# Performance work log

Hardware: AMD Instinct MI355X
Metric: run time of the kernel (lower is better)

The kernel has to match this reference:

```python
import jax, jax.numpy as jnp
import numpy as np

N_ITER = 4  # n_iter
NEG = -1e9  # masked-score fill (softmax-safe stand-in for -inf)


def _mfvi(x, mask, ternary, global_):
    """MFVI message passing between head (H) and node (Z) variables with global nodes.

    x:       [B, L, D] unary scores for Z nodes
    mask:    [B, L]    padding mask (nonzero = valid token)
    ternary: [D, D, H] ternary factor scores f(Z_i=a, Z_j=b, H-channel c)
    global_: [G, D, H] global-node factor scores
    Defaults: norm=softmax, regularize=1, stepsize=1, damping=0, async_update,
    no tensor decomposition, mode='all-attn', block_msg=False, output_prob=False.
    """
    B, L, D = x.shape
    m1 = (mask != 0)                                             # [B, L]
    pair_valid = m1[:, None, :, None] & m1[:, None, None, :]     # [B, 1, L, L]
    unary = x                                                    # pos_embed='none'
    Qz = jax.nn.softmax(unary, axis=-1)                          # [B, L, D]
    F_Z = unary
    neg = jnp.asarray(NEG, x.dtype)
    for _ in range(N_ITER):
        # --- H update: scores for head variable H_{i,c} over candidate heads j ---
        # F_Hs[n,h,i,j] = sum_{a,b} Qz[n,i,a] * ternary[a,b,h] * Qz[n,j,b]
        F_Hs = jnp.einsum('nia,abh,njb->nhij', Qz, ternary, Qz)  # [B, H, L, L]
        F_Hs = jnp.where(pair_valid, F_Hs, neg)
        # global-node columns: F_Hg[n,h,i,g] = sum_a Qz[n,i,a] * global_[g,a,h]
        F_Hg = jnp.einsum('nia,gah->nhig', Qz, global_)          # [B, H, L, G]
        F_H = jnp.concatenate([F_Hs, F_Hg], axis=-1)             # [B, H, L, L+G]
        Q_H = jax.nn.softmax(F_H, axis=-1)                       # regularize_H = 1
        Qhs, Qhg = Q_H[..., :L], Q_H[..., L:]
        # --- Z update (async: uses fresh Q_H) ---
        # message to Z_i from its chosen head j
        msg_i = jnp.einsum('nhij,njb,abh->nia', Qhs, Qz, ternary)
        # message to Z_j from dependents i (block_msg=False keeps it)
        msg_j = jnp.einsum('nhij,nia,abh->njb', Qhs, Qz, ternary)
        # message to Z_i from global nodes
        msg_g = jnp.einsum('nhig,gah->nia', Qhg, global_)
        F_Z = unary + msg_i + msg_j + msg_g                      # [B, L, D]
        Qz = jax.nn.softmax(F_Z, axis=-1)                        # regularize_Z = 1
    # output_prob=False -> unnormalized scores, zeroed at padding
    return jnp.where(m1[..., None], F_Z, jnp.zeros_like(F_Z))


def setup_inputs() -> dict:
    key = jax.random.key(0)
    k1, k2, k3 = jax.random.split(key, 3)
    B, L, D, H, G = 4, 1024, 128, 8, 64
    x = jax.random.normal(k1, (B, L, D), dtype=jnp.float32)
    mask = jnp.ones((B, L), dtype=jnp.int32)
    ternary = jax.random.normal(k2, (D, D, H), dtype=jnp.float32)          # init std=1
    global_ = jax.random.normal(k3, (G, D, H), dtype=jnp.float32) / np.sqrt(D)
    return {"x": x, "mask": mask, "ternary": ternary, "global_": global_}


def reference(x, mask, ternary, global_):
    return _mfvi(x, mask, ternary, global_)
```

## Files before the change

kernel.cpp:

```cpp
#include <hip/hip_runtime.h>
#include <math.h>

#define Bn 4
#define Ln 1024
#define Dn 128
#define Hn 8
#define Gn 64
#define NITERS 4

typedef _Float16 f16;
typedef _Float16 half8 __attribute__((ext_vector_type(8)));
typedef _Float16 half4v __attribute__((ext_vector_type(4)));
typedef float floatx4 __attribute__((ext_vector_type(4)));

#define WPAD 136
#define PPAD 72

#define MFMA(a, b, c) __builtin_amdgcn_mfma_f32_16x16x32_f16((a), (b), (c), 0, 0, 0)

__device__ __forceinline__ void gl_lds16(const f16* g, f16* l) {
    __builtin_amdgcn_global_load_lds(
        (const __attribute__((address_space(1))) void*)(g),
        (__attribute__((address_space(3))) void*)(l),
        16, 0, 0);
}

__device__ __forceinline__ void issue_tiles(const f16* us, const f16* ub, int sb,
                                            f16* UsB, f16* UbB, int w, int l) {
    #pragma unroll
    for (int k = 0; k < 4; k++) {
        int c = w * 4 + k;
        {
            int r = c * 4 + (l >> 4); int g = (l & 15) ^ (r & 7);
            gl_lds16(us + (size_t)r * Dn + g * 8, UsB + c * 512);
        }
        {
            int r = c * 8 + (l >> 3); int g = (l & 7) ^ (r & 7);
            gl_lds16(ub + (size_t)r * sb + g * 8, UbB + c * 512);
        }
    }
}

__global__ void repack_kernel(const float* __restrict__ ter, const float* __restrict__ glb,
                              f16* __restrict__ TpA, f16* __restrict__ TpB,
                              f16* __restrict__ GpA, f16* __restrict__ Gpt) {
    int idx = blockIdx.x * 256 + threadIdx.x;
    if (idx < Dn * Dn * Hn) {
        int h = idx % Hn; int b = (idx / Hn) % Dn; int a = idx / (Hn * Dn);
        f16 v = (f16)ter[idx];
        TpA[((size_t)h * Dn + a) * Dn + b] = v;
        TpB[((size_t)h * Dn + b) * Dn + a] = v;
    }
    if (idx < Gn * Dn * Hn) {
        int h = idx % Hn; int a = (idx / Hn) % Dn; int g = idx / (Hn * Dn);
        f16 v = (f16)glb[idx];
        GpA[((size_t)h * Gn + g) * Dn + a] = v;
        Gpt[((size_t)h * Dn + a) * Gn + g] = v;
    }
}

__global__ void softmax_rows_kernel(const float* __restrict__ in, f16* __restrict__ out) {
    int row = blockIdx.x;
    int t = threadIdx.x;
    __shared__ float red[2];
    float v = in[(size_t)row * Dn + t];
    float m = v;
    #pragma unroll
    for (int off = 1; off < 64; off <<= 1) m = fmaxf(m, __shfl_xor(m, off, 64));
    if ((t & 63) == 0) red[t >> 6] = m;
    __syncthreads();
    m = fmaxf(red[0], red[1]);
    float e = __expf(v - m);
    float s = e;
    #pragma unroll
    for (int off = 1; off < 64; off <<= 1) s += __shfl_xor(s, off, 64);
    __syncthreads();
    if ((t & 63) == 0) red[t >> 6] = s;
    __syncthreads();
    s = red[0] + red[1];
    out[(size_t)row * Dn + t] = (f16)(e / s);
}

__launch_bounds__(256, 4)
__global__ void uv_kernel(const f16* __restrict__ Qz, const f16* __restrict__ TpA,
                          const f16* __restrict__ TpB,
                          f16* __restrict__ U, f16* __restrict__ Ut, f16* __restrict__ Vt) {
    int bx = blockIdx.x;
    int h  = blockIdx.y;
    int n  = blockIdx.z;
    int t  = threadIdx.x;
    int w = t >> 6, l = t & 63, m = l & 15, q = l >> 4;

    __shared__ __align__(16) f16 Ts[128 * WPAD];

    int jrow = bx * 64 + w * 16 + m;
    const f16* qbase = Qz + ((size_t)n * Ln + jrow) * Dn;
    half8 aq[4];
    #pragma unroll
    for (int ks = 0; ks < 4; ks++)
        aq[ks] = *(const half8*)(qbase + ks * 32 + q * 8);

    size_t hoff = (size_t)(n * Hn + h);
    int jr0 = bx * 64 + w * 16 + 4 * q;

    {
        const f16* src = TpA + (size_t)h * Dn * Dn;
        for (int ii = 0; ii < 8; ii++) {
            int idx = t + 256 * ii; int r = idx >> 4, c = idx & 15;
            *(float4*)&Ts[r * WPAD + c * 8] = *(const float4*)(src + (size_t)r * Dn + c * 8);
        }
        __syncthreads();
        #pragma unroll
        for (int ct = 0; ct < 8; ct++) {
            floatx4 acc = {0.f, 0.f, 0.f, 0.f};
            #pragma unroll
            for (int ks = 0; ks < 4; ks++) {
                half8 b = *(const half8*)&Ts[(ct * 16 + m) * WPAD + ks * 32 + q * 8];
                acc = MFMA(aq[ks], b, acc);
            }
            f16* ub = U + (hoff * Ln + jr0) * Dn + ct * 16 + m;
            #pragma unroll
            for (int reg = 0; reg < 4; reg++) ub[(size_t)reg * Dn] = (f16)acc[reg];
            half4v pk = { (f16)acc[0], (f16)acc[1], (f16)acc[2], (f16)acc[3] };
            *(half4v*)(Ut + (hoff * Dn + ct * 16 + m) * Ln + jr0) = pk;
        }
        __syncthreads();
    }
    {
        const f16* src = TpB + (size_t)h * Dn * Dn;
        for (int ii = 0; ii < 8; ii++) {
            int idx = t + 256 * ii; int r = idx >> 4, c = idx & 15;
            *(float4*)&Ts[r * WPAD + c * 8] = *(const float4*)(src + (size_t)r * Dn + c * 8);
        }
        __syncthreads();
        #pragma unroll
        for (int ct = 0; ct < 8; ct++) {
            floatx4 acc = {0.f, 0.f, 0.f, 0.f};
            #pragma unroll
            for (int ks = 0; ks < 4; ks++) {
                half8 b = *(const half8*)&Ts[(ct * 16 + m) * WPAD + ks * 32 + q * 8];
                acc = MFMA(aq[ks], b, acc);
            }
            half4v pk = { (f16)acc[0], (f16)acc[1], (f16)acc[2], (f16)acc[3] };
            *(half4v*)(Vt + (hoff * Dn + ct * 16 + m) * Ln + jr0) = pk;
        }
    }
}

__launch_bounds__(256, 2)
__global__ void msgi_kernel(const f16* __restrict__ Qz, const f16* __restrict__ U,
                            const f16* __restrict__ Ut, const f16* __restrict__ GpA,
                            const f16* __restrict__ Gpt, const int* __restrict__ mask,
                            f16* __restrict__ Macc, float* __restrict__ rowLinv) {
    int it = blockIdx.x, h = blockIdx.y, n = blockIdx.z;
    int t = threadIdx.x;
    int w = t >> 6, l = t & 63, m = l & 15, q = l >> 4;
    int rh = w >> 1, ch = w & 1;
    int ih = w >> 1, ah = w & 1;

    __shared__ __align__(16) f16 Us[2][64 * 128];
    __shared__ __align__(16) f16 Ub[2][128 * 64];
    __shared__ __align__(16) f16 Ps[64 * PPAD];
    __shared__ int jms[2][64];
    __shared__ float lpart[2][64];
    __shared__ float linvS[64];

    half8 bq[2][4];
    #pragma unroll
    for (int ib = 0; ib < 2; ib++) {
        const f16* qr = Qz + ((size_t)n * Ln + it * 64 + ch * 32 + ib * 16 + m) * Dn;
        #pragma unroll
        for (int ks = 0; ks < 4; ks++)
            bq[ib][ks] = *(const half8*)(qr + ks * 32 + q * 8);
    }
    int im[2];
    #pragma unroll
    for (int ib = 0; ib < 2; ib++)
        im[ib] = mask[n * Ln + it * 64 + ch * 32 + ib * 16 + m];

    float lacc[2] = {0.f, 0.f};
    floatx4 Oacc[2][4];
    #pragma unroll
    for (int ib = 0; ib < 2; ib++)
        #pragma unroll
        for (int at = 0; at < 4; at++) Oacc[ib][at] = (floatx4){0.f, 0.f, 0.f, 0.f};

    size_t hoff = (size_t)(n * Hn + h);

    issue_tiles(U + hoff * Ln * Dn, Ut + hoff * Dn * Ln, Ln, Us[0], Ub[0], w, l);
    if (t < 64) jms[0][t] = mask[n * Ln + t];
    __syncthreads();

    for (int jt = 0; jt < 17; jt++) {
        int cur = jt & 1, nxt = cur ^ 1;
        if (jt + 1 < 17) {
            const f16 *us, *ub; int sb;
            if (jt + 1 < 16) {
                us = U + (hoff * Ln + (size_t)(jt + 1) * 64) * Dn;
                ub = Ut + hoff * Dn * Ln + (jt + 1) * 64;
                sb = Ln;
            } else {
                us = GpA + (size_t)h * Gn * Dn;
                ub = Gpt + (size_t)h * Dn * Gn;
                sb = Gn;
            }
            issue_tiles(us, ub, sb, Us[nxt], Ub[nxt], w, l);
            if (t < 64) jms[nxt][t] = (jt + 1 < 16) ? mask[n * Ln + (jt + 1) * 64 + t] : 1;
        }
        int isg = (jt == 16);
        #pragma unroll
        for (int jb = 0; jb < 2; jb++) {
            int r0 = rh * 32 + jb * 16 + m;
            half8 au[4];
            #pragma unroll
            for (int ks = 0; ks < 4; ks++)
                au[ks] = *(const half8*)&Us[cur][((size_t)r0 << 7) + ((((ks << 2) + q)) ^ (r0 & 7)) * 8];
            int jmr[4];
            #pragma unroll
            for (int reg = 0; reg < 4; reg++)
                jmr[reg] = jms[cur][rh * 32 + jb * 16 + 4 * q + reg];
            #pragma unroll
            for (int ib = 0; ib < 2; ib++) {
                floatx4 s = {0.f, 0.f, 0.f, 0.f};
                #pragma unroll
                for (int ks = 0; ks < 4; ks++) s = MFMA(au[ks], bq[ib][ks], s);
                half4v pk;
                #pragma unroll
                for (int reg = 0; reg < 4; reg++) {
                    float p = (isg || (im[ib] && jmr[reg])) ? __expf(fminf(s[reg], 11.f)) : 0.f;
                    lacc[ib] += p;
                    pk[reg] = (f16)p;
                }
                *(half4v*)&Ps[(ch * 32 + ib * 16 + m) * PPAD + rh * 32 + jb * 16 + 4 * q] = pk;
            }
        }
        __syncthreads();

        #pragma unroll
        for (int kst = 0; kst < 2; kst++) {
            half8 aP[2];
            #pragma unroll
            for (int ib = 0; ib < 2; ib++)
                aP[ib] = *(const half8*)&Ps[(ih * 32 + ib * 16 + m) * PPAD + kst * 32 + q * 8];
            #pragma unroll
            for (int at = 0; at < 4; at++) {
                int r0 = ah * 64 + at * 16 + m;
                half8 bU = *(const half8*)&Ub[cur][((size_t)r0 << 6) + ((((kst << 2) + q)) ^ (r0 & 7)) * 8];
                #pragma unroll
                for (int ib = 0; ib < 2; ib++)
                    Oacc[ib][at] = MFMA(aP[ib], bU, Oacc[ib][at]);
            }
        }
        __syncthreads();
    }

    #pragma unroll
    for (int ib = 0; ib < 2; ib++) {
        float v = lacc[ib];
        v += __shfl_xor(v, 16, 64);
        v += __shfl_xor(v, 32, 64);
        lacc[ib] = v;
    }
    if (q == 0) {
        lpart[rh][ch * 32 + m] = lacc[0];
        lpart[rh][ch * 32 + 16 + m] = lacc[1];
    }
    __syncthreads();
    size_t rbase = hoff * Ln + (size_t)it * 64;
    if (t < 64) {
        float inv = 1.0f / (lpart[0][t] + lpart[1][t]);
        linvS[t] = inv;
        int mk = mask[n * Ln + it * 64 + t];
        rowLinv[rbase + t] = mk ? inv : 0.f;
    }
    __syncthreads();
    f16* Mo = Macc + rbase * Dn;
    #pragma unroll
    for (int ib = 0; ib < 2; ib++)
        #pragma unroll
        for (int reg = 0; reg < 4; reg++) {
            int row = ih * 32 + ib * 16 + 4 * q + reg;
            float inv = linvS[row];
            #pragma unroll
            for (int at = 0; at < 4; at++)
                Mo[(size_t)row * Dn + ah * 64 + at * 16 + m] = (f16)(Oacc[ib][at][reg] * inv);
        }
}

__launch_bounds__(256, 2)
__global__ void msgj_kernel(const f16* __restrict__ Qz, const f16* __restrict__ U,
                            const f16* __restrict__ Vt, const int* __restrict__ mask,
                            const float* __restrict__ rowLinv, f16* __restrict__ Macc) {
    int jt = blockIdx.x, h = blockIdx.y, n = blockIdx.z;
    int t = threadIdx.x;
    int w = t >> 6, l = t & 63, m = l & 15, q = l >> 4;
    int ihs = w >> 1, jhs = w & 1;
    int jh2 = w >> 1, bh = w & 1;

    __shared__ __align__(16) f16 Qs[2][64 * 128];
    __shared__ __align__(16) f16 Vb[2][128 * 64];
    __shared__ __align__(16) f16 Psj[64 * PPAD];
    __shared__ float lvS[2][64];

    size_t hoff = (size_t)(n * Hn + h);

    half8 bu[2][4];
    #pragma unroll
    for (int jb = 0; jb < 2; jb++) {
        const f16* ur = U + (hoff * Ln + (size_t)jt * 64 + jhs * 32 + jb * 16 + m) * Dn;
        #pragma unroll
        for (int ks = 0; ks < 4; ks++)
            bu[jb][ks] = *(const half8*)(ur + ks * 32 + q * 8);
    }
    int jm[2];
    #pragma unroll
    for (int jb = 0; jb < 2; jb++)
        jm[jb] = mask[n * Ln + jt * 64 + jhs * 32 + jb * 16 + m];

    floatx4 Oacc[2][4];
    #pragma unroll
    for (int jb = 0; jb < 2; jb++)
        #pragma unroll
        for (int bt = 0; bt < 4; bt++) Oacc[jb][bt] = (floatx4){0.f, 0.f, 0.f, 0.f};

    issue_tiles(Qz + (size_t)n * Ln * Dn, Vt + hoff * Dn * Ln, Ln, Qs[0], Vb[0], w, l);
    if (t < 64) lvS[0][t] = rowLinv[hoff * Ln + t];
    __syncthreads();

    for (int it2 = 0; it2 < 16; it2++) {
        int cur = it2 & 1, nxt = cur ^ 1;
        if (it2 + 1 < 16) {
            issue_tiles(Qz + ((size_t)n * Ln + (size_t)(it2 + 1) * 64) * Dn,
                        Vt + hoff * Dn * Ln + (it2 + 1) * 64, Ln, Qs[nxt], Vb[nxt], w, l);
            if (t < 64) lvS[nxt][t] = rowLinv[hoff * Ln + (it2 + 1) * 64 + t];
        }
        #pragma unroll
        for (int ib = 0; ib < 2; ib++) {
            int r0 = ihs * 32 + ib * 16 + m;
            half8 aq2[4];
            #pragma unroll
            for (int ks = 0; ks < 4; ks++)
                aq2[ks] = *(const half8*)&Qs[cur][((size_t)r0 << 7) + ((((ks << 2) + q)) ^ (r0 & 7)) * 8];
            float lv[4];
            #pragma unroll
            for (int reg = 0; reg < 4; reg++)
                lv[reg] = lvS[cur][ihs * 32 + ib * 16 + 4 * q + reg];
            #pragma unroll
            for (int jb = 0; jb < 2; jb++) {
                floatx4 s = {0.f, 0.f, 0.f, 0.f};
                #pragma unroll
                for (int ks = 0; ks < 4; ks++) s = MFMA(aq2[ks], bu[jb][ks], s);
                half4v pk;
                #pragma unroll
                for (int reg = 0; reg < 4; reg++) {
                    float p = jm[jb] ? __expf(fminf(s[reg], 11.f)) * lv[reg] : 0.f;
                    pk[reg] = (f16)p;
                }
                *(half4v*)&Psj[(jhs * 32 + jb * 16 + m) * PPAD + ihs * 32 + ib * 16 + 4 * q] = pk;
            }
        }
        __syncthreads();

        #pragma unroll
        for (int kst = 0; kst < 2; kst++) {
            half8 aP[2];
            #pragma unroll
            for (int jb = 0; jb < 2; jb++)
                aP[jb] = *(const half8*)&Psj[(jh2 * 32 + jb * 16 + m) * PPAD + kst * 32 + q * 8];
            #pragma unroll
            for (int bt = 0; bt < 4; bt++) {
                int r0 = bh * 64 + bt * 16 + m;
                half8 bV = *(const half8*)&Vb[cur][((size_t)r0 << 6) + ((((kst << 2) + q)) ^ (r0 & 7)) * 8];
                #pragma unroll
                for (int jb = 0; jb < 2; jb++)
                    Oacc[jb][bt] = MFMA(aP[jb], bV, Oacc[jb][bt]);
            }
        }
        __syncthreads();
    }

    f16* Mo = Macc + (hoff * Ln + (size_t)jt * 64) * Dn;
    #pragma unroll
    for (int jb = 0; jb < 2; jb++)
        #pragma unroll
        for (int reg = 0; reg < 4; reg++) {
            int row = jh2 * 32 + jb * 16 + 4 * q + reg;
            #pragma unroll
            for (int bt = 0; bt < 4; bt++) {
                f16* p = &Mo[(size_t)row * Dn + bh * 64 + bt * 16 + m];
                *p = (f16)((float)*p + Oacc[jb][bt][reg]);
            }
        }
}

__global__ void combine_kernel(const float* __restrict__ x, const f16* __restrict__ Macc,
                               const int* __restrict__ mask, float* __restrict__ out,
                               f16* __restrict__ Qzh, int do_softmax, int do_mask) {
    int row = blockIdx.x;
    int t = threadIdx.x;
    __shared__ float red[2];
    int n = row >> 10;
    float acc = x[(size_t)row * Dn + t];
    const f16* mp = Macc + (size_t)n * Hn * Ln * Dn + (size_t)(row & 1023) * Dn + t;
    #pragma unroll
    for (int h = 0; h < Hn; h++) acc += (float)mp[(size_t)h * Ln * Dn];
    float o = acc;
    if (do_mask && mask[row] == 0) o = 0.f;
    out[(size_t)row * Dn + t] = o;
    if (do_softmax) {
        float m = acc;
        #pragma unroll
        for (int off = 1; off < 64; off <<= 1) m = fmaxf(m, __shfl_xor(m, off, 64));
        if ((t & 63) == 0) red[t >> 6] = m;
        __syncthreads();
        m = fmaxf(red[0], red[1]);
        float e = __expf(acc - m);
        float s = e;
        #pragma unroll
        for (int off = 1; off < 64; off <<= 1) s += __shfl_xor(s, off, 64);
        __syncthreads();
        if ((t & 63) == 0) red[t >> 6] = s;
        __syncthreads();
        s = red[0] + red[1];
        Qzh[(size_t)row * Dn + t] = (f16)(e / s);
    }
}

extern "C" void kernel_launch(void* const* d_in, const int* in_sizes, int n_in,
                              void* d_out, int out_size, void* d_ws, size_t ws_size,
                              hipStream_t stream) {
    const float* x       = (const float*)d_in[0];
    const int*   mask    = (const int*)d_in[1];
    const float* ternary = (const float*)d_in[2];
    const float* global_ = (const float*)d_in[3];
    float* out = (float*)d_out;
    (void)ws_size; (void)n_in; (void)in_sizes; (void)out_size;

    char* ws = (char*)d_ws;
    size_t o = 0;
    f16* Qzh = (f16*)(ws + o); o += (size_t)Bn * Ln * Dn * 2;
    f16* U   = (f16*)(ws + o); o += (size_t)Bn * Hn * Ln * Dn * 2;
    f16* Ut  = (f16*)(ws + o); o += (size_t)Bn * Hn * Ln * Dn * 2;
    f16* Vt  = (f16*)(ws + o); o += (size_t)Bn * Hn * Ln * Dn * 2;
    f16* TpA = (f16*)(ws + o); o += (size_t)Hn * Dn * Dn * 2;
    f16* TpB = (f16*)(ws + o); o += (size_t)Hn * Dn * Dn * 2;
    f16* GpA = (f16*)(ws + o); o += (size_t)Hn * Gn * Dn * 2;
    f16* Gpt = (f16*)(ws + o); o += (size_t)Hn * Dn * Gn * 2;
    float* rowLinv = (float*)(ws + o); o += (size_t)Bn * Hn * Ln * 4;
    f16* Macc = (f16*)(ws + o); o += (size_t)Bn * Hn * Ln * Dn * 2;

    repack_kernel<<<(Dn * Dn * Hn + 255) / 256, 256, 0, stream>>>(ternary, global_, TpA, TpB, GpA, Gpt);
    softmax_rows_kernel<<<Bn * Ln, 128, 0, stream>>>(x, Qzh);

    for (int it = 0; it < NITERS; it++) {
        uv_kernel<<<dim3(Ln / 64, Hn, Bn), 256, 0, stream>>>(Qzh, TpA, TpB, U, Ut, Vt);
        msgi_kernel<<<dim3(Ln / 64, Hn, Bn), 256, 0, stream>>>(Qzh, U, Ut, GpA, Gpt, mask, Macc, rowLinv);
        msgj_kernel<<<dim3(Ln / 64, Hn, Bn), 256, 0, stream>>>(Qzh, U, Vt, mask, rowLinv, Macc);
        combine_kernel<<<Bn * Ln, 128, 0, stream>>>(x, Macc, mask, out, Qzh,
                                                    (it < NITERS - 1) ? 1 : 0,
                                                    (it == NITERS - 1) ? 1 : 0);
    }
}
```

Before: 395.1 us.

## Load MFMA A-operand tiles directly from global instead of staging through LDS

In the msgi and msgj kernels, the U/Qz row tiles and the mask/rowLinv vectors are now read straight from global memory into registers rather than double-buffered in LDS via global_load_lds. Only the transposed B-operand tile stays staged in LDS. The uv kernel likewise reads the repacked ternary matrix directly from global instead of copying it into padded shared memory with barriers. This halves LDS use per block, which could raise occupancy, and removes staging work, but exposes global-load latency on the critical path without prefetch.

```diff
diff --git a/kernel.cpp b/kernel.cpp
--- a/kernel.cpp
+++ b/kernel.cpp
@@ -13,7 +13,6 @@
 typedef _Float16 half4v __attribute__((ext_vector_type(4)));
 typedef float floatx4 __attribute__((ext_vector_type(4)));
 
-#define WPAD 136
 #define PPAD 72
 
 #define MFMA(a, b, c) __builtin_amdgcn_mfma_f32_16x16x32_f16((a), (b), (c), 0, 0, 0)
@@ -25,19 +24,12 @@
         16, 0, 0);
 }
 
-__device__ __forceinline__ void issue_tiles(const f16* us, const f16* ub, int sb,
-                                            f16* UsB, f16* UbB, int w, int l) {
+__device__ __forceinline__ void issue_ub(const f16* ub, int sb, f16* UbB, int w, int l) {
     #pragma unroll
     for (int k = 0; k < 4; k++) {
         int c = w * 4 + k;
-        {
-            int r = c * 4 + (l >> 4); int g = (l & 15) ^ (r & 7);
-            gl_lds16(us + (size_t)r * Dn + g * 8, UsB + c * 512);
-        }
-        {
-            int r = c * 8 + (l >> 3); int g = (l & 7) ^ (r & 7);
-            gl_lds16(ub + (size_t)r * sb + g * 8, UbB + c * 512);
-        }
+        int r = c * 8 + (l >> 3); int g = (l & 7) ^ (r & 7);
+        gl_lds16(ub + (size_t)r * sb + g * 8, UbB + c * 512);
     }
 }
 
@@ -91,8 +83,6 @@
     int t  = threadIdx.x;
     int w = t >> 6, l = t & 63, m = l & 15, q = l >> 4;
 
-    __shared__ __align__(16) f16 Ts[128 * WPAD];
-
     int jrow = bx * 64 + w * 16 + m;
     const f16* qbase = Qz + ((size_t)n * Ln + jrow) * Dn;
     half8 aq[4];
@@ -105,17 +95,12 @@
 
     {
         const f16* src = TpA + (size_t)h * Dn * Dn;
-        for (int ii = 0; ii < 8; ii++) {
-            int idx = t + 256 * ii; int r = idx >> 4, c = idx & 15;
-            *(float4*)&Ts[r * WPAD + c * 8] = *(const float4*)(src + (size_t)r * Dn + c * 8);
-        }
-        __syncthreads();
         #pragma unroll
         for (int ct = 0; ct < 8; ct++) {
             floatx4 acc = {0.f, 0.f, 0.f, 0.f};
             #pragma unroll
             for (int ks = 0; ks < 4; ks++) {
-                half8 b = *(const half8*)&Ts[(ct * 16 + m) * WPAD + ks * 32 + q * 8];
+                half8 b = *(const half8*)(src + (size_t)(ct * 16 + m) * Dn + ks * 32 + q * 8);
                 acc = MFMA(aq[ks], b, acc);
             }
             f16* ub = U + (hoff * Ln + jr0) * Dn + ct * 16 + m;
@@ -124,21 +109,15 @@
             half4v pk = { (f16)acc[0], (f16)acc[1], (f16)acc[2], (f16)acc[3] };
             *(half4v*)(Ut + (hoff * Dn + ct * 16 + m) * Ln + jr0) = pk;
         }
-        __syncthreads();
     }
     {
         const f16* src = TpB + (size_t)h * Dn * Dn;
-        for (int ii = 0; ii < 8; ii++) {
-            int idx = t + 256 * ii; int r = idx >> 4, c = idx & 15;
-            *(float4*)&Ts[r * WPAD + c * 8] = *(const float4*)(src + (size_t)r * Dn + c * 8);
-        }
-        __syncthreads();
         #pragma unroll
         for (int ct = 0; ct < 8; ct++) {
             floatx4 acc = {0.f, 0.f, 0.f, 0.f};
             #pragma unroll
             for (int ks = 0; ks < 4; ks++) {
-                half8 b = *(const half8*)&Ts[(ct * 16 + m) * WPAD + ks * 32 + q * 8];
+                half8 b = *(const half8*)(src + (size_t)(ct * 16 + m) * Dn + ks * 32 + q * 8);
                 acc = MFMA(aq[ks], b, acc);
             }
             half4v pk = { (f16)acc[0], (f16)acc[1], (f16)acc[2], (f16)acc[3] };
@@ -158,10 +137,8 @@
     int rh = w >> 1, ch = w & 1;
     int ih = w >> 1, ah = w & 1;
 
-    __shared__ __align__(16) f16 Us[2][64 * 128];
     __shared__ __align__(16) f16 Ub[2][128 * 64];
     __shared__ __align__(16) f16 Ps[64 * PPAD];
-    __shared__ int jms[2][64];
     __shared__ float lpart[2][64];
     __shared__ float linvS[64];
 
@@ -187,38 +164,31 @@
 
     size_t hoff = (size_t)(n * Hn + h);
 
-    issue_tiles(U + hoff * Ln * Dn, Ut + hoff * Dn * Ln, Ln, Us[0], Ub[0], w, l);
-    if (t < 64) jms[0][t] = mask[n * Ln + t];
+    issue_ub(Ut + hoff * Dn * Ln, Ln, Ub[0], w, l);
     __syncthreads();
 
     for (int jt = 0; jt < 17; jt++) {
         int cur = jt & 1, nxt = cur ^ 1;
         if (jt + 1 < 17) {
-            const f16 *us, *ub; int sb;
-            if (jt + 1 < 16) {
-                us = U + (hoff * Ln + (size_t)(jt + 1) * 64) * Dn;
-                ub = Ut + hoff * Dn * Ln + (jt + 1) * 64;
-                sb = Ln;
-            } else {
-                us = GpA + (size_t)h * Gn * Dn;
-                ub = Gpt + (size_t)h * Dn * Gn;
-                sb = Gn;
-            }
-            issue_tiles(us, ub, sb, Us[nxt], Ub[nxt], w, l);
-            if (t < 64) jms[nxt][t] = (jt + 1 < 16) ? mask[n * Ln + (jt + 1) * 64 + t] : 1;
+            const f16* ub; int sb;
+            if (jt + 1 < 16) { ub = Ut + hoff * Dn * Ln + (jt + 1) * 64; sb = Ln; }
+            else             { ub = Gpt + (size_t)h * Dn * Gn;           sb = Gn; }
+            issue_ub(ub, sb, Ub[nxt], w, l);
         }
         int isg = (jt == 16);
+        const f16* uptr = isg ? (GpA + (size_t)h * Gn * Dn)
+                              : (U + (hoff * Ln + (size_t)jt * 64) * Dn);
         #pragma unroll
         for (int jb = 0; jb < 2; jb++) {
             int r0 = rh * 32 + jb * 16 + m;
             half8 au[4];
             #pragma unroll
             for (int ks = 0; ks < 4; ks++)
-                au[ks] = *(const half8*)&Us[cur][((size_t)r0 << 7) + ((((ks << 2) + q)) ^ (r0 & 7)) * 8];
-            int jmr[4];
-            #pragma unroll
-            for (int reg = 0; reg < 4; reg++)
-                jmr[reg] = jms[cur][rh * 32 + jb * 16 + 4 * q + reg];
+                au[ks] = *(const half8*)(uptr + (size_t)r0 * Dn + ks * 32 + q * 8);
+            int4 jmv;
+            if (isg) jmv = make_int4(1, 1, 1, 1);
+            else jmv = *(const int4*)(mask + n * Ln + jt * 64 + rh * 32 + jb * 16 + 4 * q);
+            const int* jmr = &jmv.x;
             #pragma unroll
             for (int ib = 0; ib < 2; ib++) {
                 floatx4 s = {0.f, 0.f, 0.f, 0.f};
@@ -297,10 +267,8 @@
     int ihs = w >> 1, jhs = w & 1;
     int jh2 = w >> 1, bh = w & 1;
 
-    __shared__ __align__(16) f16 Qs[2][64 * 128];
     __shared__ __align__(16) f16 Vb[2][128 * 64];
     __shared__ __align__(16) f16 Psj[64 * PPAD];
-    __shared__ float lvS[2][64];
 
     size_t hoff = (size_t)(n * Hn + h);
 
@@ -323,28 +291,23 @@
         #pragma unroll
         for (int bt = 0; bt < 4; bt++) Oacc[jb][bt] = (floatx4){0.f, 0.f, 0.f, 0.f};
 
-    issue_tiles(Qz + (size_t)n * Ln * Dn, Vt + hoff * Dn * Ln, Ln, Qs[0], Vb[0], w, l);
-    if (t < 64) lvS[0][t] = rowLinv[hoff * Ln + t];
+    issue_ub(Vt + hoff * Dn * Ln, Ln, Vb[0], w, l);
     __syncthreads();
 
     for (int it2 = 0; it2 < 16; it2++) {
         int cur = it2 & 1, nxt = cur ^ 1;
-        if (it2 + 1 < 16) {
-            issue_tiles(Qz + ((size_t)n * Ln + (size_t)(it2 + 1) * 64) * Dn,
-                        Vt + hoff * Dn * Ln + (it2 + 1) * 64, Ln, Qs[nxt], Vb[nxt], w, l);
-            if (t < 64) lvS[nxt][t] = rowLinv[hoff * Ln + (it2 + 1) * 64 + t];
-        }
+        if (it2 + 1 < 16)
+            issue_ub(Vt + hoff * Dn * Ln + (it2 + 1) * 64, Ln, Vb[nxt], w, l);
+        const f16* qptr = Qz + ((size_t)n * Ln + (size_t)it2 * 64) * Dn;
         #pragma unroll
         for (int ib = 0; ib < 2; ib++) {
             int r0 = ihs * 32 + ib * 16 + m;
             half8 aq2[4];
             #pragma unroll
             for (int ks = 0; ks < 4; ks++)
-                aq2[ks] = *(const half8*)&Qs[cur][((size_t)r0 << 7) + ((((ks << 2) + q)) ^ (r0 & 7)) * 8];
-            float lv[4];
-            #pragma unroll
-            for (int reg = 0; reg < 4; reg++)
-                lv[reg] = lvS[cur][ihs * 32 + ib * 16 + 4 * q + reg];
+                aq2[ks] = *(const half8*)(qptr + (size_t)r0 * Dn + ks * 32 + q * 8);
+            float4 lvv = *(const float4*)(rowLinv + hoff * Ln + it2 * 64 + ihs * 32 + ib * 16 + 4 * q);
+            const float* lv = &lvv.x;
             #pragma unroll
             for (int jb = 0; jb < 2; jb++) {
                 floatx4 s = {0.f, 0.f, 0.f, 0.f};
```

Result: slower. 600.0 us (+51.8%).
